# Kernel tuning notes

Measured on AMD Instinct MI355X. Metric: run time of the kernel, lower is better.

The kernel has to match this reference:

```python
import jax, jax.numpy as jnp
import numpy as np

N, E, B = 25000, 400000, 64
IN, HID, OUT, EDGE, TDIM, L = 16, 128, 16, 16, 64, 4
EIN = 2 * HID + 1 + EDGE  # 273


def _sinusoidal(t, dim):
    half = dim // 2
    freqs = jnp.exp(jnp.arange(half, dtype=jnp.float32) * (-np.log(10000.0) / (half - 1)))
    a = t[:, None] * freqs[None, :]
    return jnp.concatenate([jnp.sin(a), jnp.cos(a)], axis=-1)


def _layernorm(h, g, b, eps=1e-5):
    mu = h.mean(-1, keepdims=True)
    v = h.var(-1, keepdims=True)
    return (h - mu) / jnp.sqrt(v + eps) * g + b


def setup_inputs() -> dict:
    key = jax.random.key(0)
    ks = iter(jax.random.split(key, 64))

    def rn(shape, scale=0.05):
        return jax.random.normal(next(ks), shape, dtype=jnp.float32) * scale

    inp = {
        'h': jax.random.normal(next(ks), (N, IN), dtype=jnp.float32),
        'x': jax.random.normal(next(ks), (N, 3), dtype=jnp.float32),
        'edge_index': jax.random.randint(next(ks), (2, E), 0, N),
        't': jax.random.uniform(next(ks), (B,), dtype=jnp.float32) * 1000.0,
        'edge_attr': jax.random.normal(next(ks), (E, EDGE), dtype=jnp.float32),
        'batch': jnp.sort(jax.random.randint(next(ks), (N,), 0, B)),
        # embeddings
        'node_w': rn((IN, HID)), 'node_b': jnp.zeros((HID,), jnp.float32),
        'tw1': rn((TDIM, HID)), 'tb1': jnp.zeros((HID,), jnp.float32),
        'tw2': rn((HID, HID)), 'tb2': jnp.zeros((HID,), jnp.float32),
        # per-layer stacked params (L, ...)
        'edge_w1': rn((L, EIN, HID)), 'edge_b1': jnp.zeros((L, HID), jnp.float32),
        'edge_w2': rn((L, HID, HID)), 'edge_b2': jnp.zeros((L, HID), jnp.float32),
        'att_w': rn((L, HID, 1)), 'att_b': jnp.zeros((L, 1), jnp.float32),
        'cw1': rn((L, HID, HID)), 'cb1': jnp.zeros((L, HID), jnp.float32),
        'cw2': rn((L, HID, 1), scale=0.001),  # xavier gain=0.001
        'nw1': rn((L, 2 * HID, HID)), 'nb1': jnp.zeros((L, HID), jnp.float32),
        'nw2': rn((L, HID, HID)), 'nb2': jnp.zeros((L, HID), jnp.float32),
        'ln_g': jnp.ones((L, HID), jnp.float32), 'ln_b': jnp.zeros((L, HID), jnp.float32),
        # heads
        'out_w1': rn((HID, HID)), 'out_b1': jnp.zeros((HID,), jnp.float32),
        'out_w2': rn((HID, OUT)), 'out_b2': jnp.zeros((OUT,), jnp.float32),
        'head_w': rn((HID, 3), scale=0.01), 'head_b': jnp.zeros((3,), jnp.float32),
    }
    return inp


def reference(h, x, edge_index, t, edge_attr, batch,
              node_w, node_b, tw1, tb1, tw2, tb2,
              edge_w1, edge_b1, edge_w2, edge_b2, att_w, att_b,
              cw1, cb1, cw2, nw1, nb1, nw2, nb2, ln_g, ln_b,
              out_w1, out_b1, out_w2, out_b2, head_w, head_b):
    silu = jax.nn.silu
    n_nodes = h.shape[0]
    row, col = edge_index[0], edge_index[1]

    # node + time embedding
    h = h @ node_w + node_b
    te = _sinusoidal(t, TDIM)
    te = silu(te @ tw1 + tb1) @ tw2 + tb2
    h = h + te[batch]

    for i in range(L):
        coord_diff = x[row] - x[col]                      # (E, 3)
        radial = (coord_diff ** 2).sum(-1, keepdims=True)  # (E, 1)
        edge_in = jnp.concatenate([h[row], h[col], radial, edge_attr], axis=-1)
        m = silu(silu(edge_in @ edge_w1[i] + edge_b1[i]) @ edge_w2[i] + edge_b2[i])
        att = jax.nn.sigmoid(m @ att_w[i] + att_b[i])
        m = m * att
        cw = silu(m @ cw1[i] + cb1[i]) @ cw2[i]           # (E, 1)
        coord_diff = coord_diff / jnp.sqrt(radial + 1e-8)  # normalize=True
        x = x + jax.ops.segment_sum(coord_diff * cw, row, num_segments=n_nodes)
        m_i = jax.ops.segment_sum(m, row, num_segments=n_nodes)
        h_in = jnp.concatenate([h, m_i], axis=-1)
        h_new = h + (silu(h_in @ nw1[i] + nb1[i]) @ nw2[i] + nb2[i])
        h = _layernorm(h_new, ln_g[i], ln_b[i])

    h_out = silu(h @ out_w1 + out_b1) @ out_w2 + out_b2  # (N, OUT)
    x_out = h @ head_w + head_b                           # (N, 3)
    return h_out, x_out
```

## Files before the change

kernel.cpp:

```cpp
#include <hip/hip_runtime.h>
#include <hip/hip_bf16.h>
#include <cmath>

#define NN      25000
#define NEDGE   400000
#define NBATCH  64
#define IN_DIM  16
#define HID     128
#define OUT_DIM 16
#define EDGE_DIM 16
#define TDIM    64
#define NL      4
#define EIN     273
#define EPB     64
#define W1KB    36
#define W2KB    16
#define A_PAD   65
#define A3OFF   (16*A_PAD*8)
#define NPB     32
#define NPAD    33

typedef short bfrag __attribute__((ext_vector_type(8)));
typedef float ffrag __attribute__((ext_vector_type(4)));

__device__ __forceinline__ float siluf(float v) { return v / (1.f + __expf(-v)); }
__device__ __forceinline__ float sigm(float v)  { return 1.f / (1.f + __expf(-v)); }
__device__ __forceinline__ unsigned short f2b(float f) {
    unsigned u = __float_as_uint(f);
    u = (u + 0x7FFFu + ((u >> 16) & 1u)) >> 16;
    return (unsigned short)u;
}
__device__ __forceinline__ float b2f(unsigned short b) {
    return __uint_as_float(((unsigned)b) << 16);
}
__device__ __forceinline__ int ileave(int n) {
    return (n & 0x60) | ((n & 15) << 1) | ((n >> 4) & 1);
}

__global__ __launch_bounds__(256) void hist_kernel(const int* __restrict__ row, int* __restrict__ deg) {
    const int tid = blockIdx.x * 256 + threadIdx.x;
    if (tid < NEDGE) atomicAdd(&deg[row[tid]], 1);
}

__global__ __launch_bounds__(1024) void scan_kernel(const int* __restrict__ deg, int* __restrict__ row_start) {
    __shared__ int part[1024];
    const int tid = threadIdx.x;
    const int base = tid * 25;
    int sum = 0;
    for (int i = 0; i < 25; i++) { const int idx = base + i; if (idx < NN) sum += deg[idx]; }
    part[tid] = sum;
    __syncthreads();
    for (int off = 1; off < 1024; off <<= 1) {
        int v = (tid >= off) ? part[tid - off] : 0;
        __syncthreads();
        part[tid] += v;
        __syncthreads();
    }
    int run = part[tid] - sum;
    for (int i = 0; i < 25; i++) {
        const int idx = base + i;
        if (idx < NN) { row_start[idx] = run; run += deg[idx]; }
    }
    if (tid == 1023) row_start[NN] = part[1023];
}

__global__ __launch_bounds__(256) void scatter_kernel(
    const int* __restrict__ row, const int* __restrict__ col,
    const int* __restrict__ row_start, int* __restrict__ cursor,
    int* __restrict__ rowp, int* __restrict__ colp, int* __restrict__ eorder)
{
    const int tid = blockIdx.x * 256 + threadIdx.x;
    if (tid >= NEDGE) return;
    const int r = row[tid];
    const int pos = row_start[r] + atomicAdd(&cursor[r], 1);
    rowp[pos] = r; colp[pos] = col[tid]; eorder[pos] = tid;
}

__global__ __launch_bounds__(256) void ea_pack(
    const float* __restrict__ ea, const int* __restrict__ eorder, unsigned short* __restrict__ eabp)
{
    const int tid = blockIdx.x * 256 + threadIdx.x;
    if (tid >= NEDGE) return;
    const int e = eorder[tid];
    const float4* src = (const float4*)&ea[(size_t)e * 16];
    bfrag o0, o1;
    #pragma unroll
    for (int q = 0; q < 2; q++) {
        const float4 a = src[q];
        o0[q*4+0] = (short)f2b(a.x); o0[q*4+1] = (short)f2b(a.y);
        o0[q*4+2] = (short)f2b(a.z); o0[q*4+3] = (short)f2b(a.w);
    }
    #pragma unroll
    for (int q = 0; q < 2; q++) {
        const float4 a = src[2+q];
        o1[q*4+0] = (short)f2b(a.x); o1[q*4+1] = (short)f2b(a.y);
        o1[q*4+2] = (short)f2b(a.z); o1[q*4+3] = (short)f2b(a.w);
    }
    *(bfrag*)&eabp[(size_t)tid * 16]     = o0;
    *(bfrag*)&eabp[(size_t)tid * 16 + 8] = o1;
}

__global__ __launch_bounds__(256) void prep_w(
    const float* __restrict__ ew1, const float* __restrict__ ew2, const float* __restrict__ cw1,
    const float* __restrict__ attw,
    unsigned short* __restrict__ w1p, unsigned short* __restrict__ w2p,
    unsigned short* __restrict__ c1p, unsigned short* __restrict__ awp)
{
    const int PER_L = 70 * 128;
    int tid = blockIdx.x * 256 + threadIdx.x;
    if (tid >= NL * PER_L) return;
    const int l = tid / PER_L, rem = tid % PER_L;
    const int kb = rem >> 7, n = rem & 127;
    unsigned short o[8];
    if (kb < W1KB) {
        const float* W = ew1 + (size_t)l * EIN * HID;
        const int nc = ileave(n);
        #pragma unroll
        for (int j = 0; j < 8; j++) {
            const int k = kb * 8 + j;
            const int ok = (k < 256) ? k : (k < 272 ? k + 1 : (k == 272 ? 256 : -1));
            o[j] = (ok >= 0) ? f2b(W[(size_t)ok * HID + nc]) : (unsigned short)0;
        }
        #pragma unroll
        for (int j = 0; j < 8; j++) w1p[(((size_t)l * W1KB + kb) * 128 + n) * 8 + j] = o[j];
    } else if (kb < W1KB + W2KB) {
        const int kb2 = kb - W1KB;
        const float* W = ew2 + (size_t)l * HID * HID;
        const int nc = ileave(n);
        #pragma unroll
        for (int j = 0; j < 8; j++) o[j] = f2b(W[(size_t)(kb2 * 8 + j) * HID + nc]);
        #pragma unroll
        for (int j = 0; j < 8; j++) w2p[(((size_t)l * W2KB + kb2) * 128 + n) * 8 + j] = o[j];
    } else if (kb < W1KB + 2*W2KB) {
        const int kb2 = kb - W1KB - W2KB;
        const float* W = cw1 + (size_t)l * HID * HID;
        #pragma unroll
        for (int j = 0; j < 8; j++) o[j] = f2b(W[(size_t)(kb2 * 8 + j) * HID + n]);
        #pragma unroll
        for (int j = 0; j < 8; j++) c1p[(((size_t)l * W2KB + kb2) * 128 + n) * 8 + j] = o[j];
    } else {
        const int kbp = kb - W1KB - 2*W2KB;
        const int kbA = kbp * 8 + (n >> 4);
        const int colv = n & 15;
        const float* AWl = attw + (size_t)l * HID;
        #pragma unroll
        for (int j = 0; j < 8; j++) o[j] = f2b(AWl[kbA*8 + j]);
        #pragma unroll
        for (int j = 0; j < 8; j++) awp[(((size_t)l * 16 + kbA) * 16 + colv) * 8 + j] = o[j];
    }
}

__global__ __launch_bounds__(256) void prep_w2(
    const float* __restrict__ nw1, const float* __restrict__ nw2,
    const float* __restrict__ ow1, const float* __restrict__ ow2,
    unsigned short* __restrict__ n1p, unsigned short* __restrict__ n2p,
    unsigned short* __restrict__ o1p, unsigned short* __restrict__ o2p)
{
    const int C1 = NL * 32 * 128;
    const int C2 = C1 + NL * 16 * 128;
    const int C3 = C2 + 16 * 128;
    const int C4 = C3 + 16 * 16;
    int tid = blockIdx.x * 256 + threadIdx.x;
    if (tid >= C4) return;
    if (tid < C1) {
        const int l = tid / (32*128), rem = tid % (32*128);
        const int kb = rem >> 7, n = rem & 127;
        const int nc = ileave(n);
        #pragma unroll
        for (int j = 0; j < 8; j++)
            n1p[(size_t)tid*8 + j] = f2b(nw1[((size_t)l*256 + kb*8 + j)*128 + nc]);
    } else if (tid < C2) {
        const int t2 = tid - C1;
        const int l = t2 / (16*128), rem = t2 % (16*128);
        const int kb = rem >> 7, n = rem & 127;
        const int nc = ileave(n);
        #pragma unroll
        for (int j = 0; j < 8; j++)
            n2p[(size_t)t2*8 + j] = f2b(nw2[((size_t)l*128 + kb*8 + j)*128 + nc]);
    } else if (tid < C3) {
        const int t2 = tid - C2;
        const int kb = t2 >> 7, n = t2 & 127;
        #pragma unroll
        for (int j = 0; j < 8; j++)
            o1p[(size_t)t2*8 + j] = f2b(ow1[(size_t)(kb*8 + j)*128 + n]);
    } else {
        const int t2 = tid - C3;
        const int kb = t2 >> 4, n = t2 & 15;
        #pragma unroll
        for (int j = 0; j < 8; j++)
            o2p[(size_t)t2*8 + j] = f2b(ow2[(size_t)(kb*8 + j)*16 + n]);
    }
}

__global__ __launch_bounds__(HID) void te_kernel(
    const float* __restrict__ t, const float* __restrict__ tw1, const float* __restrict__ tb1,
    const float* __restrict__ tw2, const float* __restrict__ tb2, float* __restrict__ te_out)
{
    __shared__ float s0[TDIM];
    __shared__ float s1[HID];
    const int b = blockIdx.x, j = threadIdx.x;
    const float tv = t[b];
    if (j < TDIM) {
        const int k = j & 31;
        const float freq = expf((float)k * (-logf(10000.f) / 31.f));
        const float a = tv * freq;
        s0[j] = (j < 32) ? sinf(a) : cosf(a);
    }
    __syncthreads();
    float acc = tb1[j];
    for (int k = 0; k < TDIM; k++) acc += s0[k] * tw1[k*HID + j];
    s1[j] = siluf(acc);
    __syncthreads();
    float acc2 = tb2[j];
    for (int k = 0; k < HID; k++) acc2 += s1[k] * tw2[k*HID + j];
    te_out[b*HID + j] = acc2;
}

__global__ __launch_bounds__(256) void embed_kernel(
    const float* __restrict__ h_in, const float* __restrict__ x_in,
    const int* __restrict__ batch,
    const float* __restrict__ node_w, const float* __restrict__ node_b,
    const float* __restrict__ te, float* __restrict__ h, unsigned short* __restrict__ hbf,
    float* __restrict__ x0, float* __restrict__ m_i)
{
    __shared__ float hs[2][IN_DIM];
    const int local = threadIdx.x >> 7;
    const int j = threadIdx.x & 127;
    const int n = blockIdx.x * 2 + local;
    if (j < IN_DIM) hs[local][j] = h_in[n*IN_DIM + j];
    if (j >= 64 && j < 67) x0[n*3 + (j - 64)] = x_in[n*3 + (j - 64)];
    __syncthreads();
    float acc = node_b[j];
    #pragma unroll
    for (int k = 0; k < IN_DIM; k++) acc += hs[local][k] * node_w[k*HID + j];
    acc += te[batch[n]*HID + j];
    h[(size_t)n*HID + j]   = acc;
    hbf[(size_t)n*HID + j] = f2b(acc);
    m_i[(size_t)n*HID + j] = 0.f;
}

__global__ __launch_bounds__(256) void edge_mfma(
    const unsigned short* __restrict__ hbf, const float* __restrict__ x,
    float* __restrict__ x_new, float* __restrict__ m_i,
    const int* __restrict__ rowp, const int* __restrict__ colp,
    const unsigned short* __restrict__ eabp,
    const unsigned short* __restrict__ W1p, const float* __restrict__ B1,
    const unsigned short* __restrict__ W2p, const float* __restrict__ B2,
    const unsigned short* __restrict__ C1p, const float* __restrict__ CB1,
    const unsigned short* __restrict__ AWp, const float* __restrict__ ABv,
    const float* __restrict__ CW2)
{
    __shared__ unsigned short sA[W1KB * A_PAD * 8];
    __shared__ int rc[EPB][2];
    float* attS = (float*)sA;
    float* pscr = (float*)&sA[A3OFF];

    const int t = threadIdx.x;
    const int e0 = blockIdx.x * EPB;
    const int lane = t & 63, w = t >> 6;
    const int quad = lane >> 4, colid = lane & 15;

    float cd0 = 0.f, cd1 = 0.f, cd2 = 0.f;
    if (t < EPB) {
        const int r = rowp[e0 + t], c = colp[e0 + t];
        rc[t][0] = r; rc[t][1] = c;
        const float dx = x[r*3+0] - x[c*3+0];
        const float dy = x[r*3+1] - x[c*3+1];
        const float dz = x[r*3+2] - x[c*3+2];
        const float rad = dx*dx + dy*dy + dz*dz;
        const float inv = 1.f / sqrtf(rad + 1e-8f);
        cd0 = dx*inv; cd1 = dy*inv; cd2 = dz*inv;
        unsigned short* p34 = &sA[(34*A_PAD + t) * 8];
        p34[0] = f2b(rad);
        #pragma unroll
        for (int j = 1; j < 8; j++) p34[j] = 0;
        unsigned short* p35 = &sA[(35*A_PAD + t) * 8];
        #pragma unroll
        for (int j = 0; j < 8; j++) p35[j] = 0;
    }
    if (t < 128) {
        const int e = t >> 1, hh = t & 1;
        *(bfrag*)&sA[((32 + hh)*A_PAD + e) * 8] = *(const bfrag*)&eabp[(size_t)(e0 + e) * 16 + hh * 8];
    }
    __syncthreads();
    #pragma unroll
    for (int it = 0; it < 8; it++) {
        const int c = t + it * 256;
        const int e = (c >> 4) & 63;
        const int half = c >> 10;
        const int kb16 = c & 15;
        const int node = rc[e][half];
        *(bfrag*)&sA[((half*16 + kb16)*A_PAD + e) * 8] = *(const bfrag*)&hbf[(size_t)node * HID + kb16 * 8];
    }
    __syncthreads();

    const int f0 = w*32 + 2*colid;
    ffrag acc1[4][2];
    {
        const float b0v = B1[f0], b1v = B1[f0+1];
        #pragma unroll
        for (int mt = 0; mt < 4; mt++)
            #pragma unroll
            for (int r = 0; r < 4; r++) { acc1[mt][0][r] = b0v; acc1[mt][1][r] = b1v; }
    }
    for (int ks = 0; ks < 9; ks++) {
        const int kb = ks * 4 + quad;
        const bfrag b0 = *(const bfrag*)&W1p[((size_t)kb * 128 + w*32 + colid) * 8];
        const bfrag b1 = *(const bfrag*)&W1p[((size_t)kb * 128 + w*32 + 16 + colid) * 8];
        #pragma unroll
        for (int mt = 0; mt < 4; mt++) {
            const bfrag a = *(const bfrag*)&sA[(kb*A_PAD + mt*16 + colid) * 8];
            acc1[mt][0] = __builtin_amdgcn_mfma_f32_16x16x32_bf16(a, b0, acc1[mt][0], 0, 0, 0);
            acc1[mt][1] = __builtin_amdgcn_mfma_f32_16x16x32_bf16(a, b1, acc1[mt][1], 0, 0, 0);
        }
    }
    __syncthreads();
    {
        const int kb = f0 >> 3, j = f0 & 7;
        #pragma unroll
        for (int mt = 0; mt < 4; mt++)
            #pragma unroll
            for (int reg = 0; reg < 4; reg++) {
                const float v0 = siluf(acc1[mt][0][reg]);
                const float v1 = siluf(acc1[mt][1][reg]);
                const int e = mt*16 + quad*4 + reg;
                *(__hip_bfloat162*)&sA[(kb*A_PAD + e) * 8 + j] =
                    __float22bfloat162_rn(make_float2(v0, v1));
            }
    }
    __syncthreads();

    ffrag acc2[4][2];
    {
        const float b0v = B2[f0], b1v = B2[f0+1];
        #pragma unroll
        for (int mt = 0; mt < 4; mt++)
            #pragma unroll
            for (int r = 0; r < 4; r++) { acc2[mt][0][r] = b0v; acc2[mt][1][r] = b1v; }
    }
    for (int ks = 0; ks < 4; ks++) {
        const int kb = ks * 4 + quad;
        const bfrag b0 = *(const bfrag*)&W2p[((size_t)kb * 128 + w*32 + colid) * 8];
        const bfrag b1 = *(const bfrag*)&W2p[((size_t)kb * 128 + w*32 + 16 + colid) * 8];
        #pragma unroll
        for (int mt = 0; mt < 4; mt++) {
            const bfrag a = *(const bfrag*)&sA[(kb*A_PAD + mt*16 + colid) * 8];
            acc2[mt][0] = __builtin_amdgcn_mfma_f32_16x16x32_bf16(a, b0, acc2[mt][0], 0, 0, 0);
            acc2[mt][1] = __builtin_amdgcn_mfma_f32_16x16x32_bf16(a, b1, acc2[mt][1], 0, 0, 0);
        }
    }
    {
        const int kb = f0 >> 3, j = f0 & 7;
        #pragma unroll
        for (int mt = 0; mt < 4; mt++)
            #pragma unroll
            for (int reg = 0; reg < 4; reg++) {
                const float v0 = siluf(acc2[mt][0][reg]);
                const float v1 = siluf(acc2[mt][1][reg]);
                const int e = mt*16 + quad*4 + reg;
                *(__hip_bfloat162*)&sA[A3OFF + (kb*A_PAD + e) * 8 + j] =
                    __float22bfloat162_rn(make_float2(v0, v1));
            }
    }
    __syncthreads();

    ffrag accA;
    {
        const float abv = ABv[0];
        #pragma unroll
        for (int r = 0; r < 4; r++) accA[r] = abv;
    }
    ffrag acc3[4][2] = {};
    for (int ks = 0; ks < 4; ks++) {
        const int kb = ks * 4 + quad;
        const bfrag ab = *(const bfrag*)&AWp[((size_t)kb * 16 + colid) * 8];
        const bfrag c0 = *(const bfrag*)&C1p[((size_t)kb * 128 + w*32 + colid) * 8];
        const bfrag c1 = *(const bfrag*)&C1p[((size_t)kb * 128 + w*32 + 16 + colid) * 8];
        const bfrag aw_frag = *(const bfrag*)&sA[A3OFF + (kb*A_PAD + w*16 + colid) * 8];
        accA = __builtin_amdgcn_mfma_f32_16x16x32_bf16(aw_frag, ab, accA, 0, 0, 0);
        #pragma unroll
        for (int mt = 0; mt < 4; mt++) {
            const bfrag a = (mt == w) ? aw_frag
                : *(const bfrag*)&sA[A3OFF + (kb*A_PAD + mt*16 + colid) * 8];
            acc3[mt][0] = __builtin_amdgcn_mfma_f32_16x16x32_bf16(a, c0, acc3[mt][0], 0, 0, 0);
            acc3[mt][1] = __builtin_amdgcn_mfma_f32_16x16x32_bf16(a, c1, acc3[mt][1], 0, 0, 0);
        }
    }
    if (colid == 0) {
        #pragma unroll
        for (int reg = 0; reg < 4; reg++) attS[w*16 + quad*4 + reg] = accA[reg];
    }
    __syncthreads();
    if (t < EPB) attS[t] = sigm(attS[t]);
    __syncthreads();

    {
        const int fkb0 = lane >> 3,     fj = lane & 7;
        const int fkb1 = 8 + (lane >> 3);
        float a0 = 0.f, a1 = 0.f;
        for (int i = 0; i < 16; i++) {
            const int e = (w << 4) + i;
            const float av = attS[e];
            const int r = rc[e][0];
            a0 += b2f(sA[A3OFF + (fkb0*A_PAD + e) * 8 + fj]) * av;
            a1 += b2f(sA[A3OFF + (fkb1*A_PAD + e) * 8 + fj]) * av;
            const bool flush = (i == 15) || (rc[e+1][0] != r);
            if (flush) {
                atomicAdd(&m_i[(size_t)r * HID + lane],      a0);
                atomicAdd(&m_i[(size_t)r * HID + lane + 64], a1);
                a0 = 0.f; a1 = 0.f;
            }
        }
    }

    float p[4][4];
    {
        const float cb0v = CB1[w*32 + colid], cb1v = CB1[w*32 + 16 + colid];
        const float cwv0 = CW2[w*32 + colid], cwv1 = CW2[w*32 + 16 + colid];
        #pragma unroll
        for (int mt = 0; mt < 4; mt++) {
            const float4 a4 = *(const float4*)&attS[mt*16 + quad*4];
            const float att_r[4] = {a4.x, a4.y, a4.z, a4.w};
            #pragma unroll
            for (int reg = 0; reg < 4; reg++)
                p[mt][reg] = siluf(att_r[reg] * acc3[mt][0][reg] + cb0v) * cwv0
                           + siluf(att_r[reg] * acc3[mt][1][reg] + cb1v) * cwv1;
        }
    }
    __syncthreads();
    #pragma unroll
    for (int mt = 0; mt < 4; mt++)
        #pragma unroll
        for (int reg = 0; reg < 4; reg++)
            pscr[(mt*16 + quad*4 + reg)*68 + w*16 + colid] = p[mt][reg];
    __syncthreads();
    if (t < EPB) {
        const float* pr = pscr + t*68;
        float s = 0.f;
        #pragma unroll
        for (int k2 = 0; k2 < 16; k2++) {
            const float4 v = *(const float4*)&pr[k2*4];
            s += (v.x + v.y) + (v.z + v.w);
        }
        const int r = rc[t][0];
        atomicAdd(&x_new[r*3+0], cd0 * s);
        atomicAdd(&x_new[r*3+1], cd1 * s);
        atomicAdd(&x_new[r*3+2], cd2 * s);
    }
}

__global__ __launch_bounds__(256) void node_mfma(
    float* __restrict__ h, unsigned short* __restrict__ hbf, float* __restrict__ m_i,
    const unsigned short* __restrict__ N1p, const float* __restrict__ NB1,
    const unsigned short* __restrict__ N2p, const float* __restrict__ NB2,
    const float* __restrict__ LG, const float* __restrict__ LB)
{
    __shared__ unsigned short sA[32 * NPAD * 8];
    __shared__ float mu_s[NPB], rs_s[NPB];
    float* hres = (float*)sA;

    const int t = threadIdx.x, lane = t & 63, w = t >> 6;
    const int quad = lane >> 4, colid = lane & 15;
    const int n0 = blockIdx.x * NPB;

    #pragma unroll
    for (int it = 0; it < 2; it++) {
        const int c = t + it * 256;
        const int e = c >> 4, kb = c & 15;
        const int nidx = min(n0 + e, NN - 1);
        *(bfrag*)&sA[(kb*NPAD + e) * 8] = *(const bfrag*)&hbf[(size_t)nidx * HID + kb * 8];
    }
    #pragma unroll
    for (int it = 0; it < 2; it++) {
        const int c = t + it * 256;
        const int e = c >> 4, kb = c & 15;
        const int nidx = min(n0 + e, NN - 1);
        const float4 v0 = *(const float4*)&m_i[(size_t)nidx * HID + kb * 8];
        const float4 v1 = *(const float4*)&m_i[(size_t)nidx * HID + kb * 8 + 4];
        bfrag bv;
        bv[0]=(short)f2b(v0.x); bv[1]=(short)f2b(v0.y); bv[2]=(short)f2b(v0.z); bv[3]=(short)f2b(v0.w);
        bv[4]=(short)f2b(v1.x); bv[5]=(short)f2b(v1.y); bv[6]=(short)f2b(v1.z); bv[7]=(short)f2b(v1.w);
        *(bfrag*)&sA[((16 + kb)*NPAD + e) * 8] = bv;
        if (n0 + e < NN) {
            const float4 z4 = {0.f, 0.f, 0.f, 0.f};
            *(float4*)&m_i[(size_t)nidx * HID + kb * 8]     = z4;
            *(float4*)&m_i[(size_t)nidx * HID + kb * 8 + 4] = z4;
        }
    }
    __syncthreads();

    const int f0 = w*32 + 2*colid;
    ffrag acc1[2][2];
    {
        const float b0v = NB1[f0], b1v = NB1[f0+1];
        #pragma unroll
        for (int mt = 0; mt < 2; mt++)
            #pragma unroll
            for (int r = 0; r < 4; r++) { acc1[mt][0][r] = b0v; acc1[mt][1][r] = b1v; }
    }
    for (int ks = 0; ks < 8; ks++) {
        const int kb = ks * 4 + quad;
        const bfrag b0 = *(const bfrag*)&N1p[((size_t)kb * 128 + w*32 + colid) * 8];
        const bfrag b1 = *(const bfrag*)&N1p[((size_t)kb * 128 + w*32 + 16 + colid) * 8];
        #pragma unroll
        for (int mt = 0; mt < 2; mt++) {
            const bfrag a = *(const bfrag*)&sA[(kb*NPAD + mt*16 + colid) * 8];
            acc1[mt][0] = __builtin_amdgcn_mfma_f32_16x16x32_bf16(a, b0, acc1[mt][0], 0, 0, 0);
            acc1[mt][1] = __builtin_amdgcn_mfma_f32_16x16x32_bf16(a, b1, acc1[mt][1], 0, 0, 0);
        }
    }
    __syncthreads();
    {
        const int kb = f0 >> 3, j = f0 & 7;
        #pragma unroll
        for (int mt = 0; mt < 2; mt++)
            #pragma unroll
            for (int reg = 0; reg < 4; reg++) {
                const float v0 = siluf(acc1[mt][0][reg]);
                const float v1 = siluf(acc1[mt][1][reg]);
                const int e = mt*16 + quad*4 + reg;
                *(__hip_bfloat162*)&sA[(kb*NPAD + e) * 8 + j] =
                    __float22bfloat162_rn(make_float2(v0, v1));
            }
    }
    __syncthreads();

    ffrag acc2[2][2];
    {
        const float b0v = NB2[f0], b1v = NB2[f0+1];
        #pragma unroll
        for (int mt = 0; mt < 2; mt++)
            #pragma unroll
            for (int r = 0; r < 4; r++) { acc2[mt][0][r] = b0v; acc2[mt][1][r] = b1v; }
    }
    for (int ks = 0; ks < 4; ks++) {
        const int kb = ks * 4 + quad;
        const bfrag b0 = *(const bfrag*)&N2p[((size_t)kb * 128 + w*32 + colid) * 8];
        const bfrag b1 = *(const bfrag*)&N2p[((size_t)kb * 128 + w*32 + 16 + colid) * 8];
        #pragma unroll
        for (int mt = 0; mt < 2; mt++) {
            const bfrag a = *(const bfrag*)&sA[(kb*NPAD + mt*16 + colid) * 8];
            acc2[mt][0] = __builtin_amdgcn_mfma_f32_16x16x32_bf16(a, b0, acc2[mt][0], 0, 0, 0);
            acc2[mt][1] = __builtin_amdgcn_mfma_f32_16x16x32_bf16(a, b1, acc2[mt][1], 0, 0, 0);
        }
    }
    __syncthreads();
    {
        #pragma unroll
        for (int mt = 0; mt < 2; mt++)
            #pragma unroll
            for (int reg = 0; reg < 4; reg++) {
                const int row = mt*16 + quad*4 + reg;
                const int nidx = min(n0 + row, NN - 1);
                const float2 hr = *(const float2*)&h[(size_t)nidx*HID + f0];
                float2 o;
                o.x = acc2[mt][0][reg] + hr.x;
                o.y = acc2[mt][1][reg] + hr.y;
                *(float2*)&hres[row*130 + f0] = o;
            }
    }
    __syncthreads();
    {
        const int row = t >> 3, q = t & 7;
        float s = 0.f, s2 = 0.f;
        #pragma unroll
        for (int i = 0; i < 16; i++) {
            const float v = hres[row*130 + q*16 + i];
            s += v; s2 += v*v;
        }
        s += __shfl_xor(s, 1); s2 += __shfl_xor(s2, 1);
        s += __shfl_xor(s, 2); s2 += __shfl_xor(s2, 2);
        s += __shfl_xor(s, 4); s2 += __shfl_xor(s2, 4);
        if (q == 0) {
            const float mu = s * (1.f/HID);
            mu_s[row] = mu;
            rs_s[row] = rsqrtf(s2 * (1.f/HID) - mu*mu + 1e-5f);
        }
    }
    __syncthreads();
    for (int idx = t; idx < NPB*HID; idx += 256) {
        const int row = idx >> 7, f = idx & 127;
        const int n = n0 + row;
        if (n < NN) {
            const float v = (hres[row*130 + f] - mu_s[row]) * rs_s[row] * LG[f] + LB[f];
            h[(size_t)n*HID + f]   = v;
            hbf[(size_t)n*HID + f] = f2b(v);
        }
    }
}

__global__ __launch_bounds__(256) void out_mfma(
    const unsigned short* __restrict__ hbf,
    const unsigned short* __restrict__ O1p, const float* __restrict__ OB1,
    const unsigned short* __restrict__ O2p, const float* __restrict__ OB2,
    const float* __restrict__ HW, const float* __restrict__ HB,
    float* __restrict__ out)
{
    __shared__ unsigned short sA[32 * A_PAD * 8];
    __shared__ float hws[HID*3];
    const int A2O = 16 * A_PAD * 8;

    const int t = threadIdx.x, lane = t & 63, w = t >> 6;
    const int quad = lane >> 4, colid = lane & 15;
    const int n0 = blockIdx.x * 64;

    if (t < 128)      { hws[t] = HW[t]; hws[t+128] = HW[t+128]; }
    else if (t < 256) { const int i = t - 128 + 256; if (i < 384) hws[i] = HW[i]; }
    #pragma unroll
    for (int it = 0; it < 4; it++) {
        const int c = t + it * 256;
        const int e = c >> 4, kb = c & 15;
        const int nidx = min(n0 + e, NN - 1);
        *(bfrag*)&sA[(kb*A_PAD + e) * 8] = *(const bfrag*)&hbf[(size_t)nidx * HID + kb * 8];
    }
    __syncthreads();

    ffrag acc1[4][2];
    {
        const float b0v = OB1[w*32 + colid], b1v = OB1[w*32 + 16 + colid];
        #pragma unroll
        for (int mt = 0; mt < 4; mt++)
            #pragma unroll
            for (int r = 0; r < 4; r++) { acc1[mt][0][r] = b0v; acc1[mt][1][r] = b1v; }
    }
    for (int ks = 0; ks < 4; ks++) {
        const int kb = ks * 4 + quad;
        const bfrag b0 = *(const bfrag*)&O1p[((size_t)kb * 128 + w*32 + colid) * 8];
        const bfrag b1 = *(const bfrag*)&O1p[((size_t)kb * 128 + w*32 + 16 + colid) * 8];
        #pragma unroll
        for (int mt = 0; mt < 4; mt++) {
            const bfrag a = *(const bfrag*)&sA[(kb*A_PAD + mt*16 + colid) * 8];
            acc1[mt][0] = __builtin_amdgcn_mfma_f32_16x16x32_bf16(a, b0, acc1[mt][0], 0, 0, 0);
            acc1[mt][1] = __builtin_amdgcn_mfma_f32_16x16x32_bf16(a, b1, acc1[mt][1], 0, 0, 0);
        }
    }
    {
        #pragma unroll
        for (int mt = 0; mt < 4; mt++)
            #pragma unroll
            for (int nt = 0; nt < 2; nt++) {
                const int f = w*32 + nt*16 + colid;
                const int kb = f >> 3, j = f & 7;
                #pragma unroll
                for (int reg = 0; reg < 4; reg++) {
                    const float v = siluf(acc1[mt][nt][reg]);
                    const int e = mt*16 + quad*4 + reg;
                    sA[A2O + (kb*A_PAD + e) * 8 + j] = f2b(v);
                }
            }
    }
    __syncthreads();

    ffrag acco;
    {
        const float ob2v = OB2[colid];
        #pragma unroll
        for (int r = 0; r < 4; r++) acco[r] = ob2v;
    }
    for (int ks = 0; ks < 4; ks++) {
        const int kb = ks * 4 + quad;
        const bfrag a = *(const bfrag*)&sA[A2O + (kb*A_PAD + w*16 + colid) * 8];
        const bfrag b = *(const bfrag*)&O2p[((size_t)kb * 16 + colid) * 8];
        acco = __builtin_amdgcn_mfma_f32_16x16x32_bf16(a, b, acco, 0, 0, 0);
    }
    #pragma unroll
    for (int reg = 0; reg < 4; reg++) {
        const int rowg = w*16 + quad*4 + reg;
        const int n = n0 + rowg;
        if (n < NN) out[(size_t)n*OUT_DIM + colid] = acco[reg];
    }

    {
        const int rloc = t >> 2, q = t & 3;
        float s0 = 0.f, s1 = 0.f, s2 = 0.f;
        #pragma unroll
        for (int kk = 0; kk < 4; kk++) {
            const int kb = q*4 + kk;
            const bfrag v = *(const bfrag*)&sA[(kb*A_PAD + rloc) * 8];
            #pragma unroll
            for (int j = 0; j < 8; j++) {
                const float hv = b2f((unsigned short)v[j]);
                const int k = kb*8 + j;
                s0 += hv * hws[k*3+0]; s1 += hv * hws[k*3+1]; s2 += hv * hws[k*3+2];
            }
        }
        s0 += __shfl_xor(s0, 1); s1 += __shfl_xor(s1, 1); s2 += __shfl_xor(s2, 1);
        s0 += __shfl_xor(s0, 2); s1 += __shfl_xor(s1, 2); s2 += __shfl_xor(s2, 2);
        const int n = n0 + rloc;
        if (q == 0 && n < NN) {
            out[(size_t)NN*OUT_DIM + n*3 + 0] = s0 + HB[0];
            out[(size_t)NN*OUT_DIM + n*3 + 1] = s1 + HB[1];
            out[(size_t)NN*OUT_DIM + n*3 + 2] = s2 + HB[2];
        }
    }
}

extern "C" void kernel_launch(void* const* d_in, const int* in_sizes, int n_in,
                              void* d_out, int out_size, void* d_ws, size_t ws_size,
                              hipStream_t stream) {
    (void)in_sizes; (void)n_in; (void)out_size; (void)ws_size;
    const float* h_in      = (const float*)d_in[0];
    const float* x_in      = (const float*)d_in[1];
    const int*   edge_idx  = (const int*)  d_in[2];
    const float* t         = (const float*)d_in[3];
    const float* edge_attr = (const float*)d_in[4];
    const int*   batch     = (const int*)  d_in[5];
    const float* node_w = (const float*)d_in[6];
    const float* node_b = (const float*)d_in[7];
    const float* tw1    = (const float*)d_in[8];
    const float* tb1    = (const float*)d_in[9];
    const float* tw2    = (const float*)d_in[10];
    const float* tb2    = (const float*)d_in[11];
    const float* ew1    = (const float*)d_in[12];
    const float* eb1    = (const float*)d_in[13];
    const float* ew2    = (const float*)d_in[14];
    const float* eb2    = (const float*)d_in[15];
    const float* attw   = (const float*)d_in[16];
    const float* attb   = (const float*)d_in[17];
    const float* cw1    = (const float*)d_in[18];
    const float* cb1    = (const float*)d_in[19];
    const float* cw2    = (const float*)d_in[20];
    const float* nw1    = (const float*)d_in[21];
    const float* nb1    = (const float*)d_in[22];
    const float* nw2    = (const float*)d_in[23];
    const float* nb2    = (const float*)d_in[24];
    const float* lng    = (const float*)d_in[25];
    const float* lnb    = (const float*)d_in[26];
    const float* ow1    = (const float*)d_in[27];
    const float* ob1    = (const float*)d_in[28];
    const float* ow2    = (const float*)d_in[29];
    const float* ob2    = (const float*)d_in[30];
    const float* hw     = (const float*)d_in[31];
    const float* hb     = (const float*)d_in[32];

    const int* row = edge_idx;
    const int* col = edge_idx + NEDGE;

    float* ws  = (float*)d_ws;
    float* te  = ws;
    float* h   = te  + NBATCH*HID;
    float* m_i = h   + (size_t)NN*HID;
    float* x0  = m_i + (size_t)NN*HID;
    float* x1  = x0  + NN*3;
    unsigned short* hbf  = (unsigned short*)(x1 + NN*3);
    unsigned short* eabp = hbf + (size_t)NN*HID;
    unsigned short* w1p  = eabp + (size_t)NEDGE*EDGE_DIM;
    unsigned short* w2p  = w1p + (size_t)NL*W1KB*128*8;
    unsigned short* c1p  = w2p + (size_t)NL*W2KB*128*8;
    unsigned short* n1p  = c1p + (size_t)NL*W2KB*128*8;
    unsigned short* n2p  = n1p + (size_t)NL*32*128*8;
    unsigned short* o1p  = n2p + (size_t)NL*16*128*8;
    unsigned short* o2p  = o1p + (size_t)16*128*8;
    unsigned short* awp  = o2p + (size_t)16*16*8;
    int* deg       = (int*)(awp + (size_t)NL*16*16*8);
    int* row_start = deg + NN;
    int* cursor    = row_start + NN + 1;
    int* rowp      = cursor + NN;
    int* colp      = rowp + NEDGE;
    int* eorder    = colp + NEDGE;

    hipMemsetAsync(deg, 0, NN*sizeof(int), stream);
    hipMemsetAsync(cursor, 0, NN*sizeof(int), stream);
    hist_kernel<<<(NEDGE+255)/256, 256, 0, stream>>>(row, deg);
    scan_kernel<<<1, 1024, 0, stream>>>(deg, row_start);
    scatter_kernel<<<(NEDGE+255)/256, 256, 0, stream>>>(row, col, row_start, cursor, rowp, colp, eorder);
    ea_pack<<<(NEDGE+255)/256, 256, 0, stream>>>(edge_attr, eorder, eabp);

    prep_w<<<(NL*70*128 + 255)/256, 256, 0, stream>>>(ew1, ew2, cw1, attw, w1p, w2p, c1p, awp);
    prep_w2<<<(NL*32*128 + NL*16*128 + 16*128 + 16*16 + 255)/256, 256, 0, stream>>>(
        nw1, nw2, ow1, ow2, n1p, n2p, o1p, o2p);
    te_kernel<<<NBATCH, HID, 0, stream>>>(t, tw1, tb1, tw2, tb2, te);
    embed_kernel<<<NN/2, 256, 0, stream>>>(h_in, x_in, batch, node_w, node_b, te, h, hbf, x0, m_i);

    const int NBLK = (NN + NPB - 1) / NPB;
    const int OBLK = (NN + 63) / 64;
    float* xc = x0; float* xn = x1;
    for (int i = 0; i < NL; i++) {
        hipMemcpyAsync(xn, xc, (size_t)NN*3*sizeof(float), hipMemcpyDeviceToDevice, stream);
        edge_mfma<<<NEDGE/EPB, 256, 0, stream>>>(
            hbf, xc, xn, m_i, rowp, colp, eabp,
            w1p + (size_t)i*W1KB*128*8, eb1 + (size_t)i*HID,
            w2p + (size_t)i*W2KB*128*8, eb2 + (size_t)i*HID,
            c1p + (size_t)i*W2KB*128*8, cb1 + (size_t)i*HID,
            awp + (size_t)i*16*16*8, attb + i,
            cw2 + (size_t)i*HID);
        node_mfma<<<NBLK, 256, 0, stream>>>(
            h, hbf, m_i,
            n1p + (size_t)i*32*128*8, nb1 + (size_t)i*HID,
            n2p + (size_t)i*16*128*8, nb2 + (size_t)i*HID,
            lng + (size_t)i*HID,      lnb + (size_t)i*HID);
        float* tmp = xc; xc = xn; xn = tmp;
    }

    out_mfma<<<OBLK, 256, 0, stream>>>(hbf, o1p, ob1, o2p, ob2, hw, hb, (float*)d_out);
}
```

Before: 1.109 ms.

## Precompute per-node W1 projections P,Q and gather them instead of per-edge GEMM

The first edge-MLP matmul is split algebraically: h[row]@W1_r and h[col]@W1_c are computed once per node in a new pq_kernel, stored as bf16 P and Q, and gathered per edge. Only the 17-wide radial and edge-attribute part stays as a small per-edge MFMA. The attention dot product moves from MFMA to a scalar LDS reduction, and the coordinate partial sums use wave shuffles instead of a large LDS scratch. This removes most per-edge first-layer MFMA work and the hbf gathers, at the cost of an extra kernel per layer and an extra bf16 rounding of P and Q.

```diff
diff --git a/kernel.cpp b/kernel.cpp
--- a/kernel.cpp
+++ b/kernel.cpp
@@ -13,7 +13,6 @@
 #define NL      4
 #define EIN     273
 #define EPB     64
-#define W1KB    36
 #define W2KB    16
 #define A_PAD   65
 #define A3OFF   (16*A_PAD*8)
@@ -102,51 +101,56 @@
 
 __global__ __launch_bounds__(256) void prep_w(
     const float* __restrict__ ew1, const float* __restrict__ ew2, const float* __restrict__ cw1,
-    const float* __restrict__ attw,
-    unsigned short* __restrict__ w1p, unsigned short* __restrict__ w2p,
-    unsigned short* __restrict__ c1p, unsigned short* __restrict__ awp)
-{
-    const int PER_L = 70 * 128;
+    unsigned short* __restrict__ w1x, unsigned short* __restrict__ w1rp,
+    unsigned short* __restrict__ w1cp, unsigned short* __restrict__ w2p,
+    unsigned short* __restrict__ c1p)
+{
+    const int PER_L = 68 * 128;
     int tid = blockIdx.x * 256 + threadIdx.x;
     if (tid >= NL * PER_L) return;
     const int l = tid / PER_L, rem = tid % PER_L;
     const int kb = rem >> 7, n = rem & 127;
     unsigned short o[8];
-    if (kb < W1KB) {
-        const float* W = ew1 + (size_t)l * EIN * HID;
+    const float* W1 = ew1 + (size_t)l * EIN * HID;
+    if (kb < 4) {
         const int nc = ileave(n);
         #pragma unroll
         for (int j = 0; j < 8; j++) {
-            const int k = kb * 8 + j;
-            const int ok = (k < 256) ? k : (k < 272 ? k + 1 : (k == 272 ? 256 : -1));
-            o[j] = (ok >= 0) ? f2b(W[(size_t)ok * HID + nc]) : (unsigned short)0;
-        }
-        #pragma unroll
-        for (int j = 0; j < 8; j++) w1p[(((size_t)l * W1KB + kb) * 128 + n) * 8 + j] = o[j];
-    } else if (kb < W1KB + W2KB) {
-        const int kb2 = kb - W1KB;
+            const int kk = kb * 8 + j;
+            const int ok = (kk < 16) ? (257 + kk) : (kk == 16 ? 256 : -1);
+            o[j] = (ok >= 0) ? f2b(W1[(size_t)ok * HID + nc]) : (unsigned short)0;
+        }
+        #pragma unroll
+        for (int j = 0; j < 8; j++) w1x[(((size_t)l * 4 + kb) * 128 + n) * 8 + j] = o[j];
+    } else if (kb < 20) {
+        const int kb2 = kb - 4;
+        const int nc = ileave(n);
+        #pragma unroll
+        for (int j = 0; j < 8; j++) o[j] = f2b(W1[(size_t)(kb2 * 8 + j) * HID + nc]);
+        #pragma unroll
+        for (int j = 0; j < 8; j++) w1rp[(((size_t)l * 16 + kb2) * 128 + n) * 8 + j] = o[j];
+    } else if (kb < 36) {
+        const int kb2 = kb - 20;
+        const int nc = ileave(n);
+        #pragma unroll
+        for (int j = 0; j < 8; j++) o[j] = f2b(W1[(size_t)(128 + kb2 * 8 + j) * HID + nc]);
+        #pragma unroll
+        for (int j = 0; j < 8; j++) w1cp[(((size_t)l * 16 + kb2) * 128 + n) * 8 + j] = o[j];
+    } else if (kb < 52) {
+        const int kb2 = kb - 36;
         const float* W = ew2 + (size_t)l * HID * HID;
         const int nc = ileave(n);
         #pragma unroll
         for (int j = 0; j < 8; j++) o[j] = f2b(W[(size_t)(kb2 * 8 + j) * HID + nc]);
         #pragma unroll
         for (int j = 0; j < 8; j++) w2p[(((size_t)l * W2KB + kb2) * 128 + n) * 8 + j] = o[j];
-    } else if (kb < W1KB + 2*W2KB) {
-        const int kb2 = kb - W1KB - W2KB;
+    } else {
+        const int kb2 = kb - 52;
         const float* W = cw1 + (size_t)l * HID * HID;
         #pragma unroll
         for (int j = 0; j < 8; j++) o[j] = f2b(W[(size_t)(kb2 * 8 + j) * HID + n]);
         #pragma unroll
         for (int j = 0; j < 8; j++) c1p[(((size_t)l * W2KB + kb2) * 128 + n) * 8 + j] = o[j];
-    } else {
-        const int kbp = kb - W1KB - 2*W2KB;
-        const int kbA = kbp * 8 + (n >> 4);
-        const int colv = n & 15;
-        const float* AWl = attw + (size_t)l * HID;
-        #pragma unroll
-        for (int j = 0; j < 8; j++) o[j] = f2b(AWl[kbA*8 + j]);
-        #pragma unroll
-        for (int j = 0; j < 8; j++) awp[(((size_t)l * 16 + kbA) * 16 + colv) * 8 + j] = o[j];
     }
 }
 
@@ -239,26 +243,80 @@
     m_i[(size_t)n*HID + j] = 0.f;
 }
 
+__global__ __launch_bounds__(256) void pq_kernel(
+    const unsigned short* __restrict__ hbf,
+    const unsigned short* __restrict__ Wr, const unsigned short* __restrict__ Wc,
+    unsigned short* __restrict__ P, unsigned short* __restrict__ Q)
+{
+    __shared__ unsigned short sA[16 * A_PAD * 8];
+    const int t = threadIdx.x, lane = t & 63, w = t >> 6;
+    const int quad = lane >> 4, colid = lane & 15;
+    const int n0 = blockIdx.x * 64;
+
+    #pragma unroll
+    for (int it = 0; it < 4; it++) {
+        const int c = t + it * 256;
+        const int e = c >> 4, kb = c & 15;
+        const int nidx = min(n0 + e, NN - 1);
+        *(bfrag*)&sA[(kb*A_PAD + e) * 8] = *(const bfrag*)&hbf[(size_t)nidx * HID + kb * 8];
+    }
+    __syncthreads();
+
+    ffrag aP[4][2] = {}, aQ[4][2] = {};
+    for (int ks = 0; ks < 4; ks++) {
+        const int kb = ks * 4 + quad;
+        const bfrag p0 = *(const bfrag*)&Wr[((size_t)kb * 128 + w*32 + colid) * 8];
+        const bfrag p1 = *(const bfrag*)&Wr[((size_t)kb * 128 + w*32 + 16 + colid) * 8];
+        const bfrag q0 = *(const bfrag*)&Wc[((size_t)kb * 128 + w*32 + colid) * 8];
+        const bfrag q1 = *(const bfrag*)&Wc[((size_t)kb * 128 + w*32 + 16 + colid) * 8];
+        #pragma unroll
+        for (int mt = 0; mt < 4; mt++) {
+            const bfrag a = *(const bfrag*)&sA[(kb*A_PAD + mt*16 + colid) * 8];
+            aP[mt][0] = __builtin_amdgcn_mfma_f32_16x16x32_bf16(a, p0, aP[mt][0], 0, 0, 0);
+            aP[mt][1] = __builtin_amdgcn_mfma_f32_16x16x32_bf16(a, p1, aP[mt][1], 0, 0, 0);
+            aQ[mt][0] = __builtin_amdgcn_mfma_f32_16x16x32_bf16(a, q0, aQ[mt][0], 0, 0, 0);
+            aQ[mt][1] = __builtin_amdgcn_mfma_f32_16x16x32_bf16(a, q1, aQ[mt][1], 0, 0, 0);
+        }
+    }
+    const int f0 = w*32 + 2*colid;
+    #pragma unroll
+    for (int mt = 0; mt < 4; mt++)
+        #pragma unroll
+        for (int reg = 0; reg < 4; reg++) {
+            const int n = n0 + mt*16 + quad*4 + reg;
+            if (n < NN) {
+                *(__hip_bfloat162*)&P[(size_t)n*HID + f0] =
+                    __float22bfloat162_rn(make_float2(aP[mt][0][reg], aP[mt][1][reg]));
+                *(__hip_bfloat162*)&Q[(size_t)n*HID + f0] =
+                    __float22bfloat162_rn(make_float2(aQ[mt][0][reg], aQ[mt][1][reg]));
+            }
+        }
+}
+
 __global__ __launch_bounds__(256) void edge_mfma(
-    const unsigned short* __restrict__ hbf, const float* __restrict__ x,
+    const unsigned short* __restrict__ P, const unsigned short* __restrict__ Q,
+    const float* __restrict__ x,
     float* __restrict__ x_new, float* __restrict__ m_i,
     const int* __restrict__ rowp, const int* __restrict__ colp,
     const unsigned short* __restrict__ eabp,
-    const unsigned short* __restrict__ W1p, const float* __restrict__ B1,
+    const unsigned short* __restrict__ W1X, const float* __restrict__ B1,
     const unsigned short* __restrict__ W2p, const float* __restrict__ B2,
     const unsigned short* __restrict__ C1p, const float* __restrict__ CB1,
-    const unsigned short* __restrict__ AWp, const float* __restrict__ ABv,
+    const float* __restrict__ AW, const float* __restrict__ ABv,
     const float* __restrict__ CW2)
 {
-    __shared__ unsigned short sA[W1KB * A_PAD * 8];
+    __shared__ unsigned short sA[32 * A_PAD * 8];
     __shared__ int rc[EPB][2];
-    float* attS = (float*)sA;
-    float* pscr = (float*)&sA[A3OFF];
+    __shared__ float AWs[HID];
+    float* scr   = (float*)sA;
+    float* attS  = scr;
+    float* cpart = scr + 64;
 
     const int t = threadIdx.x;
     const int e0 = blockIdx.x * EPB;
     const int lane = t & 63, w = t >> 6;
     const int quad = lane >> 4, colid = lane & 15;
+    const int f0 = w*32 + 2*colid;
 
     float cd0 = 0.f, cd1 = 0.f, cd2 = 0.f;
     if (t < EPB) {
@@ -270,74 +328,66 @@
         const float rad = dx*dx + dy*dy + dz*dz;
         const float inv = 1.f / sqrtf(rad + 1e-8f);
         cd0 = dx*inv; cd1 = dy*inv; cd2 = dz*inv;
-        unsigned short* p34 = &sA[(34*A_PAD + t) * 8];
-        p34[0] = f2b(rad);
-        #pragma unroll
-        for (int j = 1; j < 8; j++) p34[j] = 0;
-        unsigned short* p35 = &sA[(35*A_PAD + t) * 8];
-        #pragma unroll
-        for (int j = 0; j < 8; j++) p35[j] = 0;
-    }
+        unsigned short* p2 = &sA[A3OFF + (2*A_PAD + t) * 8];
+        p2[0] = f2b(rad);
+        #pragma unroll
+        for (int j = 1; j < 8; j++) p2[j] = 0;
+        unsigned short* p3 = &sA[A3OFF + (3*A_PAD + t) * 8];
+        #pragma unroll
+        for (int j = 0; j < 8; j++) p3[j] = 0;
+    }
+    if (t >= 128 && t < 256) AWs[t - 128] = AW[t - 128];
     if (t < 128) {
         const int e = t >> 1, hh = t & 1;
-        *(bfrag*)&sA[((32 + hh)*A_PAD + e) * 8] = *(const bfrag*)&eabp[(size_t)(e0 + e) * 16 + hh * 8];
-    }
-    __syncthreads();
-    #pragma unroll
-    for (int it = 0; it < 8; it++) {
-        const int c = t + it * 256;
-        const int e = (c >> 4) & 63;
-        const int half = c >> 10;
-        const int kb16 = c & 15;
-        const int node = rc[e][half];
-        *(bfrag*)&sA[((half*16 + kb16)*A_PAD + e) * 8] = *(const bfrag*)&hbf[(size_t)node * HID + kb16 * 8];
-    }
-    __syncthreads();
-
-    const int f0 = w*32 + 2*colid;
-    ffrag acc1[4][2];
+        *(bfrag*)&sA[A3OFF + (hh*A_PAD + e) * 8] = *(const bfrag*)&eabp[(size_t)(e0 + e) * 16 + hh * 8];
+    }
+    __syncthreads();
+
+    ffrag accea[4][2];
     {
         const float b0v = B1[f0], b1v = B1[f0+1];
         #pragma unroll
         for (int mt = 0; mt < 4; mt++)
             #pragma unroll
-            for (int r = 0; r < 4; r++) { acc1[mt][0][r] = b0v; acc1[mt][1][r] = b1v; }
-    }
-    for (int ks = 0; ks < 9; ks++) {
-        const int kb = ks * 4 + quad;
-        const bfrag b0 = *(const bfrag*)&W1p[((size_t)kb * 128 + w*32 + colid) * 8];
-        const bfrag b1 = *(const bfrag*)&W1p[((size_t)kb * 128 + w*32 + 16 + colid) * 8];
+            for (int r = 0; r < 4; r++) { accea[mt][0][r] = b0v; accea[mt][1][r] = b1v; }
+    }
+    {
+        const bfrag eb0 = *(const bfrag*)&W1X[((size_t)quad * 128 + w*32 + colid) * 8];
+        const bfrag eb1 = *(const bfrag*)&W1X[((size_t)quad * 128 + w*32 + 16 + colid) * 8];
         #pragma unroll
         for (int mt = 0; mt < 4; mt++) {
-            const bfrag a = *(const bfrag*)&sA[(kb*A_PAD + mt*16 + colid) * 8];
-            acc1[mt][0] = __builtin_amdgcn_mfma_f32_16x16x32_bf16(a, b0, acc1[mt][0], 0, 0, 0);
-            acc1[mt][1] = __builtin_amdgcn_mfma_f32_16x16x32_bf16(a, b1, acc1[mt][1], 0, 0, 0);
-        }
-    }
-    __syncthreads();
+            const bfrag a = *(const bfrag*)&sA[A3OFF + (quad*A_PAD + mt*16 + colid) * 8];
+            accea[mt][0] = __builtin_amdgcn_mfma_f32_16x16x32_bf16(a, eb0, accea[mt][0], 0, 0, 0);
+            accea[mt][1] = __builtin_amdgcn_mfma_f32_16x16x32_bf16(a, eb1, accea[mt][1], 0, 0, 0);
+        }
+    }
+
     {
         const int kb = f0 >> 3, j = f0 & 7;
         #pragma unroll
-        for (int mt = 0; mt < 4; mt++)
+        for (int mt = 0; mt < 4; mt++) {
+            unsigned pv[4], qv[4];
             #pragma unroll
             for (int reg = 0; reg < 4; reg++) {
-                const float v0 = siluf(acc1[mt][0][reg]);
-                const float v1 = siluf(acc1[mt][1][reg]);
                 const int e = mt*16 + quad*4 + reg;
+                pv[reg] = *(const unsigned*)&P[(size_t)rc[e][0]*HID + f0];
+                qv[reg] = *(const unsigned*)&Q[(size_t)rc[e][1]*HID + f0];
+            }
+            #pragma unroll
+            for (int reg = 0; reg < 4; reg++) {
+                const int e = mt*16 + quad*4 + reg;
+                const float v0 = siluf(__uint_as_float(pv[reg] << 16)
+                                     + __uint_as_float(qv[reg] << 16) + accea[mt][0][reg]);
+                const float v1 = siluf(__uint_as_float(pv[reg] & 0xFFFF0000u)
+                                     + __uint_as_float(qv[reg] & 0xFFFF0000u) + accea[mt][1][reg]);
                 *(__hip_bfloat162*)&sA[(kb*A_PAD + e) * 8 + j] =
                     __float22bfloat162_rn(make_float2(v0, v1));
             }
-    }
-    __syncthreads();
-
-    ffrag acc2[4][2];
-    {
-        const float b0v = B2[f0], b1v = B2[f0+1];
-        #pragma unroll
-        for (int mt = 0; mt < 4; mt++)
-            #pragma unroll
-            for (int r = 0; r < 4; r++) { acc2[mt][0][r] = b0v; acc2[mt][1][r] = b1v; }
-    }
+        }
+    }
+    __syncthreads();
+
+    ffrag acc2[4][2] = {};
     for (int ks = 0; ks < 4; ks++) {
         const int kb = ks * 4 + quad;
         const bfrag b0 = *(const bfrag*)&W2p[((size_t)kb * 128 + w*32 + colid) * 8];
@@ -351,12 +401,13 @@
     }
     {
         const int kb = f0 >> 3, j = f0 & 7;
+        const float b0v = B2[f0], b1v = B2[f0+1];
         #pragma unroll
         for (int mt = 0; mt < 4; mt++)
             #pragma unroll
             for (int reg = 0; reg < 4; reg++) {
-                const float v0 = siluf(acc2[mt][0][reg]);
-                const float v1 = siluf(acc2[mt][1][reg]);
+                const float v0 = siluf(acc2[mt][0][reg] + b0v);
+                const float v1 = siluf(acc2[mt][1][reg] + b1v);
                 const int e = mt*16 + quad*4 + reg;
                 *(__hip_bfloat162*)&sA[A3OFF + (kb*A_PAD + e) * 8 + j] =
                     __float22bfloat162_rn(make_float2(v0, v1));
@@ -364,35 +415,34 @@
     }
     __syncthreads();
 
-    ffrag accA;
-    {
-        const float abv = ABv[0];
-        #pragma unroll
-        for (int r = 0; r < 4; r++) accA[r] = abv;
-    }
+    {
+        const int e = t >> 2, q = t & 3;
+        float s = 0.f;
+        #pragma unroll
+        for (int kk = 0; kk < 4; kk++) {
+            const int kb = q*4 + kk;
+            const bfrag v = *(const bfrag*)&sA[A3OFF + (kb*A_PAD + e) * 8];
+            #pragma unroll
+            for (int j = 0; j < 8; j++) s += b2f((unsigned short)v[j]) * AWs[kb*8 + j];
+        }
+        s += __shfl_xor(s, 1);
+        s += __shfl_xor(s, 2);
+        if (q == 0) attS[e] = sigm(s + ABv[0]);
+    }
+    __syncthreads();
+
     ffrag acc3[4][2] = {};
     for (int ks = 0; ks < 4; ks++) {
         const int kb = ks * 4 + quad;
-        const bfrag ab = *(const bfrag*)&AWp[((size_t)kb * 16 + colid) * 8];
-        const bfrag c0 = *(const bfrag*)&C1p[((size_t)kb * 128 + w*32 + colid) * 8];
-        const bfrag c1 = *(const bfrag*)&C1p[((size_t)kb * 128 + w*32 + 16 + colid) * 8];
-        const bfrag aw_frag = *(const bfrag*)&sA[A3OFF + (kb*A_PAD + w*16 + colid) * 8];
-        accA = __builtin_amdgcn_mfma_f32_16x16x32_bf16(aw_frag, ab, accA, 0, 0, 0);
+        const bfrag b0 = *(const bfrag*)&C1p[((size_t)kb * 128 + w*32 + colid) * 8];
+        const bfrag b1 = *(const bfrag*)&C1p[((size_t)kb * 128 + w*32 + 16 + colid) * 8];
         #pragma unroll
         for (int mt = 0; mt < 4; mt++) {
-            const bfrag a = (mt == w) ? aw_frag
-                : *(const bfrag*)&sA[A3OFF + (kb*A_PAD + mt*16 + colid) * 8];
-            acc3[mt][0] = __builtin_amdgcn_mfma_f32_16x16x32_bf16(a, c0, acc3[mt][0], 0, 0, 0);
-            acc3[mt][1] = __builtin_amdgcn_mfma_f32_16x16x32_bf16(a, c1, acc3[mt][1], 0, 0, 0);
-        }
-    }
-    if (colid == 0) {
-        #pragma unroll
-        for (int reg = 0; reg < 4; reg++) attS[w*16 + quad*4 + reg] = accA[reg];
-    }
-    __syncthreads();
-    if (t < EPB) attS[t] = sigm(attS[t]);
-    __syncthreads();
+            const bfrag a = *(const bfrag*)&sA[A3OFF + (kb*A_PAD + mt*16 + colid) * 8];
+            acc3[mt][0] = __builtin_amdgcn_mfma_f32_16x16x32_bf16(a, b0, acc3[mt][0], 0, 0, 0);
+            acc3[mt][1] = __builtin_amdgcn_mfma_f32_16x16x32_bf16(a, b1, acc3[mt][1], 0, 0, 0);
+        }
+    }
 
     {
         const int fkb0 = lane >> 3,     fj = lane & 7;
@@ -413,35 +463,38 @@
         }
     }
 
-    float p[4][4];
     {
         const float cb0v = CB1[w*32 + colid], cb1v = CB1[w*32 + 16 + colid];
         const float cwv0 = CW2[w*32 + colid], cwv1 = CW2[w*32 + 16 + colid];
+        float att_r[4][4];
         #pragma unroll
         for (int mt = 0; mt < 4; mt++) {
             const float4 a4 = *(const float4*)&attS[mt*16 + quad*4];
-            const float att_r[4] = {a4.x, a4.y, a4.z, a4.w};
+            att_r[mt][0] = a4.x; att_r[mt][1] = a4.y; att_r[mt][2] = a4.z; att_r[mt][3] = a4.w;
+        }
+        float p[4][4];
+        #pragma unroll
+        for (int mt = 0; mt < 4; mt++)
             #pragma unroll
             for (int reg = 0; reg < 4; reg++)
-                p[mt][reg] = siluf(att_r[reg] * acc3[mt][0][reg] + cb0v) * cwv0
-                           + siluf(att_r[reg] * acc3[mt][1][reg] + cb1v) * cwv1;
-        }
-    }
-    __syncthreads();
-    #pragma unroll
-    for (int mt = 0; mt < 4; mt++)
-        #pragma unroll
-        for (int reg = 0; reg < 4; reg++)
-            pscr[(mt*16 + quad*4 + reg)*68 + w*16 + colid] = p[mt][reg];
+                p[mt][reg] = siluf(att_r[mt][reg] * acc3[mt][0][reg] + cb0v) * cwv0
+                           + siluf(att_r[mt][reg] * acc3[mt][1][reg] + cb1v) * cwv1;
+        __syncthreads();
+        #pragma unroll
+        for (int mt = 0; mt < 4; mt++)
+            #pragma unroll
+            for (int reg = 0; reg < 4; reg++) {
+                float s = p[mt][reg];
+                s += __shfl_xor(s, 1);
+                s += __shfl_xor(s, 2);
+                s += __shfl_xor(s, 4);
+                s += __shfl_xor(s, 8);
+                if (colid == 0) cpart[(mt*16 + quad*4 + reg) * 4 + w] = s;
+            }
+    }
     __syncthreads();
     if (t < EPB) {
-        const float* pr = pscr + t*68;
-        float s = 0.f;
-        #pragma unroll
-        for (int k2 = 0; k2 < 16; k2++) {
-            const float4 v = *(const float4*)&pr[k2*4];
-            s += (v.x + v.y) + (v.z + v.w);
-        }
+        const float s = cpart[t*4+0] + cpart[t*4+1] + cpart[t*4+2] + cpart[t*4+3];
         const int r = rc[t][0];
         atomicAdd(&x_new[r*3+0], cd0 * s);
         atomicAdd(&x_new[r*3+1], cd1 * s);
@@ -744,15 +797,18 @@
     float* x1  = x0  + NN*3;
     unsigned short* hbf  = (unsigned short*)(x1 + NN*3);
     unsigned short* eabp = hbf + (size_t)NN*HID;
-    unsigned short* w1p  = eabp + (size_t)NEDGE*EDGE_DIM;
-    unsigned short* w2p  = w1p + (size_t)NL*W1KB*128*8;
-    unsigned short* c1p  = w2p + (size_t)NL*W2KB*128*8;
-    unsigned short* n1p  = c1p + (size_t)NL*W2KB*128*8;
-    unsigned short* n2p  = n1p + (size_t)NL*32*128*8;
-    unsigned short* o1p  = n2p + (size_t)NL*16*128*8;
-    unsigned short* o2p  = o1p + (size_t)16*128*8;
-    unsigned short* awp  = o2p + (size_t)16*16*8;
-    int* deg       = (int*)(awp + (size_t)NL*16*16*8);
+    unsigned short* w1x  = eabp + (size_t)NEDGE*EDGE_DIM;
+    unsigned short* w1rp = w1x  + (size_t)NL*4*128*8;
+    unsigned short* w1cp = w1rp + (size_t)NL*16*128*8;
+    unsigned short* w2p  = w1cp + (size_t)NL*16*128*8;
+    unsigned short* c1p  = w2p  + (size_t)NL*16*128*8;
+    unsigned short* n1p  = c1p  + (size_t)NL*16*128*8;
+    unsigned short* n2p  = n1p  + (size_t)NL*32*128*8;
+    unsigned short* o1p  = n2p  + (size_t)NL*16*128*8;
+    unsigned short* o2p  = o1p  + (size_t)16*128*8;
+    unsigned short* Pq   = o2p  + (size_t)16*16*8;
+    unsigned short* Qq   = Pq   + (size_t)NN*HID;
+    int* deg       = (int*)(Qq + (size_t)NN*HID);
     int* row_start = deg + NN;
     int* cursor    = row_start + NN + 1;
     int* rowp      = cursor + NN;
@@ -766,7 +822,7 @@
     scatter_kernel<<<(NEDGE+255)/256, 256, 0, stream>>>(row, col, row_start, cursor, rowp, colp, eorder);
     ea_pack<<<(NEDGE+255)/256, 256, 0, stream>>>(edge_attr, eorder, eabp);
 
-    prep_w<<<(NL*70*128 + 255)/256, 256, 0, stream>>>(ew1, ew2, cw1, attw, w1p, w2p, c1p, awp);
+    prep_w<<<(NL*68*128 + 255)/256, 256, 0, stream>>>(ew1, ew2, cw1, w1x, w1rp, w1cp, w2p, c1p);
     prep_w2<<<(NL*32*128 + NL*16*128 + 16*128 + 16*16 + 255)/256, 256, 0, stream>>>(
         nw1, nw2, ow1, ow2, n1p, n2p, o1p, o2p);
     te_kernel<<<NBATCH, HID, 0, stream>>>(t, tw1, tb1, tw2, tb2, te);
@@ -776,13 +832,15 @@
     const int OBLK = (NN + 63) / 64;
     float* xc = x0; float* xn = x1;
     for (int i = 0; i < NL; i++) {
+        pq_kernel<<<OBLK, 256, 0, stream>>>(
+            hbf, w1rp + (size_t)i*16*128*8, w1cp + (size_t)i*16*128*8, Pq, Qq);
         hipMemcpyAsync(xn, xc, (size_t)NN*3*sizeof(float), hipMemcpyDeviceToDevice, stream);
         edge_mfma<<<NEDGE/EPB, 256, 0, stream>>>(
-            hbf, xc, xn, m_i, rowp, colp, eabp,
-            w1p + (size_t)i*W1KB*128*8, eb1 + (size_t)i*HID,
-            w2p + (size_t)i*W2KB*128*8, eb2 + (size_t)i*HID,
-            c1p + (size_t)i*W2KB*128*8, cb1 + (size_t)i*HID,
-            awp + (size_t)i*16*16*8, attb + i,
+            Pq, Qq, xc, xn, m_i, rowp, colp, eabp,
+            w1x + (size_t)i*4*128*8, eb1 + (size_t)i*HID,
+            w2p + (size_t)i*16*128*8, eb2 + (size_t)i*HID,
+            c1p + (size_t)i*16*128*8, cb1 + (size_t)i*HID,
+            attw + (size_t)i*HID, attb + i,
             cw2 + (size_t)i*HID);
         node_mfma<<<NBLK, 256, 0, stream>>>(
             h, hbf, m_i,
```

Result: faster. 1.077 ms (-2.9%).
